# Performance work log

Measured on AMD Instinct MI355X. Metric: run time of the kernel, lower is better.

Reference implementation:

```python
import jax, jax.numpy as jnp
import numpy as np

N, E, F, H, G = 50000, 640000, 128, 128, 64


def setup_inputs() -> dict:
    key = jax.random.key(0)
    ks = jax.random.split(key, 10)
    x = jax.random.normal(ks[0], (N, F), dtype=jnp.float32)
    edge_index = jax.random.randint(ks[1], (2, E), 0, N)
    batch = jnp.sort(jax.random.randint(ks[2], (N,), 0, G))

    def glorot(k, shp):
        return jax.random.normal(k, shp, dtype=jnp.float32) * np.float32(1.0 / np.sqrt(shp[0]))

    W1 = glorot(ks[3], (F, H)); b1 = jnp.zeros((H,), jnp.float32)
    W2 = glorot(ks[4], (H, H)); b2 = jnp.zeros((H,), jnp.float32)
    W3 = glorot(ks[5], (H, H)); b3 = jnp.zeros((H,), jnp.float32)
    W4 = glorot(ks[6], (H, 2)); b4 = jnp.zeros((2,), jnp.float32)
    return {"x": x, "W1": W1, "b1": b1, "W2": W2, "b2": b2,
            "W3": W3, "b3": b3, "W4": W4, "b4": b4,
            "edge_index": edge_index, "batch": batch, "num_graphs": G}


def reference(x, W1, b1, W2, b2, W3, b3, W4, b4, edge_index, batch, num_graphs):
    n = x.shape[0]
    loop = jnp.arange(n, dtype=edge_index.dtype)
    src = jnp.concatenate([edge_index[0], loop])  # with self-loops (PyG GCNConv default)
    dst = jnp.concatenate([edge_index[1], loop])
    # symmetric degree normalization: D^{-1/2} (A+I) D^{-1/2}
    deg = jax.ops.segment_sum(jnp.ones_like(src, dtype=x.dtype), dst, num_segments=n)
    dinv = jnp.where(deg > 0, jax.lax.rsqrt(deg), 0.0)
    norm = (dinv[src] * dinv[dst])[:, None]  # [E+N, 1]

    def gcn_conv(h, W, b):
        m = h @ W                                   # transform first (F->H), then propagate
        agg = jax.ops.segment_sum(m[src] * norm, dst, num_segments=n)
        return agg + b

    h = jax.nn.relu(gcn_conv(x, W1, b1))
    h = jax.nn.relu(gcn_conv(h, W2, b2))
    g = jax.ops.segment_max(h, batch, num_segments=num_graphs)  # global_max_pool
    z = jax.nn.relu(g @ W3 + b3)                    # dropout is identity in eval
    logits = z @ W4 + b4
    return jax.nn.log_softmax(logits, axis=1)
```

## Files before the change

kernel.cpp:

```cpp
#include <hip/hip_runtime.h>
#include <hip/hip_bf16.h>
#include <math.h>

#define HDIM 128
#define SCAN_B 256
#define NBLK 256

typedef short bfrag __attribute__((ext_vector_type(8)));
typedef float f32x4 __attribute__((ext_vector_type(4)));

__device__ inline unsigned short f2bf_rne(float x) {
    unsigned u = __float_as_uint(x);
    u = (u + 0x7fffu + ((u >> 16) & 1u)) >> 16;
    return (unsigned short)u;
}
__device__ inline float bf_lo(unsigned u) { return __uint_as_float(u << 16); }
__device__ inline float bf_hi(unsigned u) { return __uint_as_float(u & 0xffff0000u); }
__device__ inline unsigned bf_pack(float lo, float hi) {
    return ((unsigned)f2bf_rne(hi) << 16) | (unsigned)f2bf_rne(lo);
}


__device__ inline void hist_body(int b, const int* __restrict__ dst,
                                 int* __restrict__ hist, int E, int chunk, int nbuck) {
    __shared__ int hl[256];
    int t = threadIdx.x;
    hl[t] = 0;
    __syncthreads();
    int start = b * chunk, end = min(E, start + chunk);
    for (int e = start + t; e < end; e += 256) atomicAdd(&hl[dst[e] >> 8], 1);
    __syncthreads();
    if (t < nbuck) hist[t * NBLK + b] = hl[t];
}

__device__ inline void wfrag_body(int b, const float* __restrict__ W1,
                                  const float* __restrict__ W2,
                                  unsigned short* __restrict__ w1h,
                                  unsigned short* __restrict__ w1l,
                                  unsigned short* __restrict__ w2h,
                                  unsigned short* __restrict__ w2l) {
    const float* W = (b < 64) ? W1 : W2;
    unsigned short* whi = (b < 64) ? w1h : w2h;
    unsigned short* wlo = (b < 64) ? w1l : w2l;
    int idx = (b & 63) * 256 + threadIdx.x;
    int k = idx >> 7;
    int n = idx & 127;
    int kt = k >> 5, q = (k >> 3) & 3, j = k & 7;
    int lm = n >> 3, nt = n & 7;
    int lane = q * 16 + lm;
    int o = ((kt * 8 + nt) * 64 + lane) * 8 + j;
    float x = W[idx];
    unsigned short hb = f2bf_rne(x);
    float hf = __uint_as_float(((unsigned)hb) << 16);
    unsigned short lb = f2bf_rne(x - hf);
    whi[o] = hb;
    wlo[o] = lb;
}

__device__ inline void scatter_body(int b, const int* __restrict__ srcv,
                                    const int* __restrict__ dstv,
                                    const int* __restrict__ hscan,
                                    int2* __restrict__ sorted,
                                    int E, int chunk, int nbuck) {
    __shared__ int cur[256];
    int t = threadIdx.x;
    if (t < nbuck) cur[t] = hscan[t * NBLK + b];
    __syncthreads();
    int start = b * chunk, end = min(E, start + chunk);
    for (int e = start + t; e < end; e += 256) {
        int d = dstv[e];
        int pos = atomicAdd(&cur[d >> 8], 1);
        sorted[pos] = make_int2(srcv[e], d);
    }
}

#define GBM 64
__device__ inline void gemm_f32_body(int b, const float* __restrict__ A,
                                     const unsigned short* __restrict__ whi,
                                     const unsigned short* __restrict__ wlo,
                                     unsigned short* __restrict__ C, int Nrows) {
    int tid = threadIdx.x;
    int w = tid >> 6, L = tid & 63;
    int lm = L & 15, lq = L >> 4;
    int row0 = b * GBM + w * 16;

    f32x4 acc[8];
#pragma unroll
    for (int nt = 0; nt < 8; ++nt) acc[nt] = (f32x4)(0.f);

#pragma unroll
    for (int kt = 0; kt < 4; ++kt) {
        int gr = row0 + lm;
        float4 v0 = make_float4(0.f, 0.f, 0.f, 0.f);
        float4 v1 = v0;
        if (gr < Nrows) {
            const float* p = &A[(size_t)gr * HDIM + kt * 32 + lq * 8];
            v0 = *(const float4*)p;
            v1 = *(const float4*)(p + 4);
        }
        float xv[8] = {v0.x, v0.y, v0.z, v0.w, v1.x, v1.y, v1.z, v1.w};
        bfrag ah, al;
#pragma unroll
        for (int j = 0; j < 8; ++j) {
            float x = xv[j];
            unsigned short hb = f2bf_rne(x);
            float hf = __uint_as_float(((unsigned)hb) << 16);
            unsigned short lb = f2bf_rne(x - hf);
            ah[j] = (short)hb;
            al[j] = (short)lb;
        }
#pragma unroll
        for (int nt = 0; nt < 8; ++nt) {
            int o = ((kt * 8 + nt) * 64 + L) * 8;
            bfrag wh = *(const bfrag*)&whi[o];
            bfrag wl = *(const bfrag*)&wlo[o];
            acc[nt] = __builtin_amdgcn_mfma_f32_16x16x32_bf16(ah, wh, acc[nt], 0, 0, 0);
            acc[nt] = __builtin_amdgcn_mfma_f32_16x16x32_bf16(al, wh, acc[nt], 0, 0, 0);
            acc[nt] = __builtin_amdgcn_mfma_f32_16x16x32_bf16(ah, wl, acc[nt], 0, 0, 0);
        }
    }

#pragma unroll
    for (int i = 0; i < 4; ++i) {
        int gr = row0 + lq * 4 + i;
        if (gr < Nrows) {
            bfrag e;
#pragma unroll
            for (int nt = 0; nt < 8; ++nt) e[nt] = (short)f2bf_rne(acc[nt][i]);
            *(bfrag*)&C[(size_t)gr * HDIM + lm * 8] = e;
        }
    }
}

__global__ __launch_bounds__(256) void mega1_kernel(const int* __restrict__ dst,
                                                    int* __restrict__ hist, int E,
                                                    int chunk, int nbuck,
                                                    const float* __restrict__ W1,
                                                    const float* __restrict__ W2,
                                                    unsigned short* __restrict__ w1h,
                                                    unsigned short* __restrict__ w1l,
                                                    unsigned short* __restrict__ w2h,
                                                    unsigned short* __restrict__ w2l) {
    int b = blockIdx.x;
    if (b < NBLK) hist_body(b, dst, hist, E, chunk, nbuck);
    else wfrag_body(b - NBLK, W1, W2, w1h, w1l, w2h, w2l);
}

__global__ __launch_bounds__(256) void mega3_kernel(const int* __restrict__ srcv,
                                                    const int* __restrict__ dstv,
                                                    const int* __restrict__ hscan,
                                                    int2* __restrict__ sorted,
                                                    int E, int chunk, int nbuck,
                                                    const float* __restrict__ A,
                                                    const unsigned short* __restrict__ whi,
                                                    const unsigned short* __restrict__ wlo,
                                                    unsigned short* __restrict__ C, int Nrows) {
    int b = blockIdx.x;
    if (b < NBLK) scatter_body(b, srcv, dstv, hscan, sorted, E, chunk, nbuck);
    else gemm_f32_body(b - NBLK, A, whi, wlo, C, Nrows);
}

__global__ __launch_bounds__(SCAN_B) void scan1_kernel(const int* __restrict__ in,
                                                       int* __restrict__ out,
                                                       int* __restrict__ sums, int n) {
    __shared__ int s[SCAN_B];
    int t = threadIdx.x;
    int idx = blockIdx.x * SCAN_B + t;
    int v = (idx < n) ? in[idx] : 0;
    s[t] = v;
    __syncthreads();
    for (int off = 1; off < SCAN_B; off <<= 1) {
        int x = (t >= off) ? s[t - off] : 0;
        __syncthreads();
        s[t] += x;
        __syncthreads();
    }
    if (idx < n) out[idx] = s[t];
    if (t == SCAN_B - 1) sums[blockIdx.x] = s[t];
}

__global__ __launch_bounds__(SCAN_B) void scan2_kernel(int* __restrict__ sums, int nb) {
    __shared__ int s[SCAN_B];
    int t = threadIdx.x;
    int v = (t < nb) ? sums[t] : 0;
    s[t] = v;
    __syncthreads();
    for (int off = 1; off < SCAN_B; off <<= 1) {
        int x = (t >= off) ? s[t - off] : 0;
        __syncthreads();
        s[t] += x;
        __syncthreads();
    }
    if (t < nb) sums[t] = s[t] - v;
}

__global__ __launch_bounds__(SCAN_B) void scan3_kernel(const int* __restrict__ in,
                                                       int* __restrict__ out,
                                                       const int* __restrict__ sums, int n) {
    int idx = blockIdx.x * SCAN_B + threadIdx.x;
    if (idx < n) out[idx] = out[idx] - in[idx] + sums[blockIdx.x];
}

__global__ __launch_bounds__(256) void csr_kernel(const int2* __restrict__ sorted,
                                                  const int* __restrict__ hscan,
                                                  int* __restrict__ rowstart,
                                                  float* __restrict__ dinv,
                                                  int* __restrict__ csr,
                                                  int N, int E, int nbuck) {
    __shared__ int cnt[256];
    __shared__ int s[256];
    __shared__ int cur[256];
    int b = blockIdx.x;
    int t = threadIdx.x;
    int start = hscan[b * NBLK];
    int end = (b + 1 < nbuck) ? hscan[(b + 1) * NBLK] : E;
    cnt[t] = 0;
    __syncthreads();
    for (int e = start + t; e < end; e += 256)
        atomicAdd(&cnt[sorted[e].y & 255], 1);
    __syncthreads();
    int v = cnt[t];
    s[t] = v;
    __syncthreads();
    for (int off = 1; off < 256; off <<= 1) {
        int x = (t >= off) ? s[t - off] : 0;
        __syncthreads();
        s[t] += x;
        __syncthreads();
    }
    int excl = s[t] - v;
    int node = b * 256 + t;
    if (node < N) {
        rowstart[node] = start + excl;
        dinv[node] = rsqrtf((float)(v + 1));
    }
    if (b == nbuck - 1 && t == 0) rowstart[N] = E;
    cur[t] = start + excl;
    __syncthreads();
    for (int e = start + t; e < end; e += 256) {
        int2 ed = sorted[e];
        int pos = atomicAdd(&cur[ed.y & 255], 1);
        csr[pos] = ed.x;
    }
}

#define QACC(UV, WT)                                   \
    acc[0] = fmaf(WT, bf_lo((UV).x), acc[0]);          \
    acc[1] = fmaf(WT, bf_hi((UV).x), acc[1]);          \
    acc[2] = fmaf(WT, bf_lo((UV).y), acc[2]);          \
    acc[3] = fmaf(WT, bf_hi((UV).y), acc[3]);          \
    acc[4] = fmaf(WT, bf_lo((UV).z), acc[4]);          \
    acc[5] = fmaf(WT, bf_hi((UV).z), acc[5]);          \
    acc[6] = fmaf(WT, bf_lo((UV).w), acc[6]);          \
    acc[7] = fmaf(WT, bf_hi((UV).w), acc[7]);

__device__ inline void qgather(const uint4* __restrict__ m4,
                               const int* __restrict__ csr,
                               const float* __restrict__ dinv,
                               int p, int pend, int t, float* acc) {
    for (; p + 8 <= pend; p += 8) {
        int s0 = csr[p], s1 = csr[p + 1], s2 = csr[p + 2], s3 = csr[p + 3];
        int s4 = csr[p + 4], s5 = csr[p + 5], s6 = csr[p + 6], s7 = csr[p + 7];
        float w0 = dinv[s0], w1 = dinv[s1], w2 = dinv[s2], w3 = dinv[s3];
        float w4 = dinv[s4], w5 = dinv[s5], w6 = dinv[s6], w7 = dinv[s7];
        uint4 u0 = m4[(size_t)s0 * 16 + t];
        uint4 u1 = m4[(size_t)s1 * 16 + t];
        uint4 u2 = m4[(size_t)s2 * 16 + t];
        uint4 u3 = m4[(size_t)s3 * 16 + t];
        uint4 u4 = m4[(size_t)s4 * 16 + t];
        uint4 u5 = m4[(size_t)s5 * 16 + t];
        uint4 u6 = m4[(size_t)s6 * 16 + t];
        uint4 u7 = m4[(size_t)s7 * 16 + t];
        QACC(u0, w0); QACC(u1, w1); QACC(u2, w2); QACC(u3, w3);
        QACC(u4, w4); QACC(u5, w5); QACC(u6, w6); QACC(u7, w7);
    }
    if (p + 4 <= pend) {
        int s0 = csr[p], s1 = csr[p + 1], s2 = csr[p + 2], s3 = csr[p + 3];
        float w0 = dinv[s0], w1 = dinv[s1], w2 = dinv[s2], w3 = dinv[s3];
        uint4 u0 = m4[(size_t)s0 * 16 + t];
        uint4 u1 = m4[(size_t)s1 * 16 + t];
        uint4 u2 = m4[(size_t)s2 * 16 + t];
        uint4 u3 = m4[(size_t)s3 * 16 + t];
        QACC(u0, w0); QACC(u1, w1); QACC(u2, w2); QACC(u3, w3);
        p += 4;
    }
    if (p + 2 <= pend) {
        int s0 = csr[p], s1 = csr[p + 1];
        float w0 = dinv[s0], w1 = dinv[s1];
        uint4 u0 = m4[(size_t)s0 * 16 + t];
        uint4 u1 = m4[(size_t)s1 * 16 + t];
        QACC(u0, w0); QACC(u1, w1);
        p += 2;
    }
    if (p < pend) {
        int s0 = csr[p];
        float w0 = dinv[s0];
        uint4 u0 = m4[(size_t)s0 * 16 + t];
        QACC(u0, w0);
    }
}

__global__ __launch_bounds__(256) void agg_gemm_kernel(
        const uint4* __restrict__ m4,
        const int* __restrict__ rowstart,
        const int* __restrict__ csr,
        const float* __restrict__ dinv,
        const float* __restrict__ bias,
        const unsigned short* __restrict__ whi,
        const unsigned short* __restrict__ wlo,
        uint4* __restrict__ out_m, int n) {
    __shared__ unsigned short hbuf[16][HDIM + 8];
    __shared__ float cbuf[16][HDIM + 4];
    int t = threadIdx.x & 15;
    int nl = threadIdx.x >> 4;
    int node = blockIdx.x * 16 + nl;

    unsigned short hv[8] = {0, 0, 0, 0, 0, 0, 0, 0};
    if (node < n) {
        float dd = dinv[node];
        float acc[8];
        uint4 u = m4[(size_t)node * 16 + t];
        acc[0] = dd * bf_lo(u.x); acc[1] = dd * bf_hi(u.x);
        acc[2] = dd * bf_lo(u.y); acc[3] = dd * bf_hi(u.y);
        acc[4] = dd * bf_lo(u.z); acc[5] = dd * bf_hi(u.z);
        acc[6] = dd * bf_lo(u.w); acc[7] = dd * bf_hi(u.w);
        qgather(m4, csr, dinv, rowstart[node], rowstart[node + 1], t, acc);
        float4 b0 = *(const float4*)&bias[t * 8];
        float4 b1 = *(const float4*)&bias[t * 8 + 4];
        float bb[8] = {b0.x, b0.y, b0.z, b0.w, b1.x, b1.y, b1.z, b1.w};
#pragma unroll
        for (int j = 0; j < 8; ++j)
            hv[j] = f2bf_rne(fmaxf(fmaf(dd, acc[j], bb[j]), 0.f));
    }
    *(uint4*)&hbuf[nl][t * 8] = *(uint4*)hv;
    __syncthreads();

    int w = threadIdx.x >> 6, L = threadIdx.x & 63;
    int lm = L & 15, lq = L >> 4;
    f32x4 acc2[2];
    acc2[0] = (f32x4)(0.f);
    acc2[1] = (f32x4)(0.f);
#pragma unroll
    for (int kt = 0; kt < 4; ++kt) {
        bfrag a = *(const bfrag*)&hbuf[lm][kt * 32 + lq * 8];
#pragma unroll
        for (int q2 = 0; q2 < 2; ++q2) {
            int nt = w * 2 + q2;
            int o = ((kt * 8 + nt) * 64 + L) * 8;
            bfrag wh = *(const bfrag*)&whi[o];
            bfrag wl = *(const bfrag*)&wlo[o];
            acc2[q2] = __builtin_amdgcn_mfma_f32_16x16x32_bf16(a, wh, acc2[q2], 0, 0, 0);
            acc2[q2] = __builtin_amdgcn_mfma_f32_16x16x32_bf16(a, wl, acc2[q2], 0, 0, 0);
        }
    }
#pragma unroll
    for (int q2 = 0; q2 < 2; ++q2) {
        int nt = w * 2 + q2;
#pragma unroll
        for (int i = 0; i < 4; ++i) cbuf[lq * 4 + i][lm * 8 + nt] = acc2[q2][i];
    }
    __syncthreads();

    if (node < n) {
        float4 r0 = *(const float4*)&cbuf[nl][t * 8];
        float4 r1 = *(const float4*)&cbuf[nl][t * 8 + 4];
        unsigned short ev[8];
        ev[0] = f2bf_rne(r0.x); ev[1] = f2bf_rne(r0.y);
        ev[2] = f2bf_rne(r0.z); ev[3] = f2bf_rne(r0.w);
        ev[4] = f2bf_rne(r1.x); ev[5] = f2bf_rne(r1.y);
        ev[6] = f2bf_rne(r1.z); ev[7] = f2bf_rne(r1.w);
        out_m[(size_t)node * 16 + t] = *(uint4*)ev;
    }
}

__global__ __launch_bounds__(256) void agg_pool_kernel(const uint4* __restrict__ m4,
                                                       const int* __restrict__ rowstart,
                                                       const int* __restrict__ csr,
                                                       const float* __restrict__ dinv,
                                                       const float* __restrict__ bias,
                                                       const int* __restrict__ batch,
                                                       unsigned int* __restrict__ g, int n) {
    __shared__ float smx[16][HDIM];
    __shared__ int sgid[16];
    int t = threadIdx.x & 15;
    int nl = threadIdx.x >> 4;
    int node = blockIdx.x * 16 + nl;
    bool valid = node < n;
    if (valid) {
        float dd = dinv[node];
        float acc[8];
        uint4 u = m4[(size_t)node * 16 + t];
        acc[0] = dd * bf_lo(u.x); acc[1] = dd * bf_hi(u.x);
        acc[2] = dd * bf_lo(u.y); acc[3] = dd * bf_hi(u.y);
        acc[4] = dd * bf_lo(u.z); acc[5] = dd * bf_hi(u.z);
        acc[6] = dd * bf_lo(u.w); acc[7] = dd * bf_hi(u.w);
        qgather(m4, csr, dinv, rowstart[node], rowstart[node + 1], t, acc);
        float4 b0 = *(const float4*)&bias[t * 8];
        float4 b1 = *(const float4*)&bias[t * 8 + 4];
        float4 r0, r1;
        r0.x = fmaxf(fmaf(dd, acc[0], b0.x), 0.f);
        r0.y = fmaxf(fmaf(dd, acc[1], b0.y), 0.f);
        r0.z = fmaxf(fmaf(dd, acc[2], b0.z), 0.f);
        r0.w = fmaxf(fmaf(dd, acc[3], b0.w), 0.f);
        r1.x = fmaxf(fmaf(dd, acc[4], b1.x), 0.f);
        r1.y = fmaxf(fmaf(dd, acc[5], b1.y), 0.f);
        r1.z = fmaxf(fmaf(dd, acc[6], b1.z), 0.f);
        r1.w = fmaxf(fmaf(dd, acc[7], b1.w), 0.f);
        *(float4*)&smx[nl][t * 8] = r0;
        *(float4*)&smx[nl][t * 8 + 4] = r1;
    }
    if (t == 0) sgid[nl] = valid ? batch[node] : -1;
    __syncthreads();
    if (threadIdx.x < HDIM) {
        int c = threadIdx.x;
        int curg = -1;
        float run = 0.f;
#pragma unroll
        for (int r = 0; r < 16; ++r) {
            int gg = sgid[r];
            if (gg < 0) continue;
            if (gg != curg) {
                if (curg >= 0) atomicMax(&g[curg * HDIM + c], __float_as_uint(run));
                curg = gg;
                run = smx[r][c];
            } else {
                run = fmaxf(run, smx[r][c]);
            }
        }
        if (curg >= 0) atomicMax(&g[curg * HDIM + c], __float_as_uint(run));
    }
}

__global__ __launch_bounds__(128) void mlp_kernel(const unsigned int* __restrict__ gbits,
                                                  const float* __restrict__ W3,
                                                  const float* __restrict__ b3,
                                                  const float* __restrict__ W4,
                                                  const float* __restrict__ b4,
                                                  float* __restrict__ out) {
    __shared__ float gs[HDIM];
    __shared__ float r0[HDIM];
    __shared__ float r1[HDIM];
    int j = threadIdx.x;
    int b = blockIdx.x;
    gs[j] = __uint_as_float(gbits[b * HDIM + j]);
    __syncthreads();
    float acc = b3[j];
#pragma unroll 8
    for (int k = 0; k < HDIM; ++k) acc = fmaf(gs[k], W3[k * HDIM + j], acc);
    float z = fmaxf(acc, 0.f);
    r0[j] = z * W4[j * 2 + 0];
    r1[j] = z * W4[j * 2 + 1];
    __syncthreads();
    for (int off = 64; off > 0; off >>= 1) {
        if (j < off) {
            r0[j] += r0[j + off];
            r1[j] += r1[j + off];
        }
        __syncthreads();
    }
    if (j == 0) {
        float l0 = r0[0] + b4[0];
        float l1 = r1[0] + b4[1];
        float mx = fmaxf(l0, l1);
        float lse = mx + logf(expf(l0 - mx) + expf(l1 - mx));
        out[b * 2 + 0] = l0 - lse;
        out[b * 2 + 1] = l1 - lse;
    }
}

extern "C" void kernel_launch(void* const* d_in, const int* in_sizes, int n_in,
                              void* d_out, int out_size, void* d_ws, size_t ws_size,
                              hipStream_t stream) {
    const float* x  = (const float*)d_in[0];
    const float* W1 = (const float*)d_in[1];
    const float* b1 = (const float*)d_in[2];
    const float* W2 = (const float*)d_in[3];
    const float* b2 = (const float*)d_in[4];
    const float* W3 = (const float*)d_in[5];
    const float* b3 = (const float*)d_in[6];
    const float* W4 = (const float*)d_in[7];
    const float* b4 = (const float*)d_in[8];
    const int* ei    = (const int*)d_in[9];
    const int* batch = (const int*)d_in[10];

    const int N = in_sizes[0] / HDIM;
    const int E = in_sizes[9] / 2;
    const int G = out_size / 2;
    const int* src = ei;
    const int* dst = ei + E;

    const int nbuck = (N + 255) >> 8;
    const int nscan = nbuck * NBLK;
    const int chunk = (E + NBLK - 1) / NBLK;

    const int Nr = ((N + 63) / 64) * 64;
    char* wsb = (char*)d_ws;
    size_t o = 0;
    unsigned int* g = (unsigned int*)(wsb + o); o += (size_t)G * HDIM * 4;
    size_t zero_bytes = o;
    int* hist = (int*)(wsb + o);           o += (size_t)nscan * 4;
    int* hscan = (int*)(wsb + o);          o += (size_t)nscan * 4;
    int* sums = (int*)(wsb + o);           o += 256 * 4;
    int* rowstart = (int*)(wsb + o);       o += (size_t)(Nr + 64) * 4;
    float* dinv = (float*)(wsb + o);       o += (size_t)Nr * 4;
    int2* sorted = (int2*)(wsb + o);       o += (size_t)E * 8;
    int* csr = (int*)(wsb + o);            o += (size_t)E * 4;
    unsigned short* wf1h = (unsigned short*)(wsb + o); o += (size_t)HDIM * HDIM * 2;
    unsigned short* wf1l = (unsigned short*)(wsb + o); o += (size_t)HDIM * HDIM * 2;
    unsigned short* wf2h = (unsigned short*)(wsb + o); o += (size_t)HDIM * HDIM * 2;
    unsigned short* wf2l = (unsigned short*)(wsb + o); o += (size_t)HDIM * HDIM * 2;
    unsigned short* m = (unsigned short*)(wsb + o);    o += (size_t)Nr * HDIM * 2;
    unsigned short* m2 = (unsigned short*)(wsb + o);   o += (size_t)Nr * HDIM * 2;
    (void)ws_size; (void)n_in;

    (void)hipMemsetAsync(d_ws, 0, zero_bytes, stream);

    int sblocks = (nscan + SCAN_B - 1) / SCAN_B;
    int gemm_blocks = (N + GBM - 1) / GBM;
    int agg_blocks = (N + 15) / 16;

    mega1_kernel<<<NBLK + 128, 256, 0, stream>>>(dst, hist, E, chunk, nbuck,
                                                 W1, W2, wf1h, wf1l, wf2h, wf2l);
    scan1_kernel<<<sblocks, SCAN_B, 0, stream>>>(hist, hscan, sums, nscan);
    scan2_kernel<<<1, SCAN_B, 0, stream>>>(sums, sblocks);
    scan3_kernel<<<sblocks, SCAN_B, 0, stream>>>(hist, hscan, sums, nscan);
    mega3_kernel<<<NBLK + gemm_blocks, 256, 0, stream>>>(src, dst, hscan, sorted,
                                                         E, chunk, nbuck,
                                                         x, wf1h, wf1l, m, N);
    csr_kernel<<<nbuck, 256, 0, stream>>>(sorted, hscan, rowstart, dinv, csr, N, E, nbuck);
    agg_gemm_kernel<<<agg_blocks, 256, 0, stream>>>((const uint4*)m, rowstart, csr,
                                                    dinv, b1, wf2h, wf2l,
                                                    (uint4*)m2, N);
    agg_pool_kernel<<<agg_blocks, 256, 0, stream>>>((const uint4*)m2, rowstart, csr,
                                                    dinv, b2, batch, g, N);
    mlp_kernel<<<G, 128, 0, stream>>>(g, W3, b3, W4, b4, (float*)d_out);
}
```

Before: 201.7 us.

## Pack sorted edges into 32-bit words, fuse scan passes, alias LDS buffers

The bucketed edge list now stores the source index and the low 8 bits of the destination in one 32-bit int instead of an int2, halving scatter and CSR traffic. The scan2 and scan3 kernels are merged so that each block re-scans the block sums itself, removing one launch. In agg_gemm, the bf16 staging buffer and the fp32 output buffer now share one LDS array, with an extra barrier between uses. The packing assumes source indices fit in 16 bits, but N=50000 needs them to fit in 65536, which holds only for this size.

After: 202.8 us. No clear change (+0.5%).

```diff
diff --git a/kernel.cpp b/kernel.cpp
--- a/kernel.cpp
+++ b/kernel.cpp
@@ -16,9 +16,6 @@
 }
 __device__ inline float bf_lo(unsigned u) { return __uint_as_float(u << 16); }
 __device__ inline float bf_hi(unsigned u) { return __uint_as_float(u & 0xffff0000u); }
-__device__ inline unsigned bf_pack(float lo, float hi) {
-    return ((unsigned)f2bf_rne(hi) << 16) | (unsigned)f2bf_rne(lo);
-}
 
 
 __device__ inline void hist_body(int b, const int* __restrict__ dst,
@@ -60,7 +57,7 @@
 __device__ inline void scatter_body(int b, const int* __restrict__ srcv,
                                     const int* __restrict__ dstv,
                                     const int* __restrict__ hscan,
-                                    int2* __restrict__ sorted,
+                                    int* __restrict__ sorted,
                                     int E, int chunk, int nbuck) {
     __shared__ int cur[256];
     int t = threadIdx.x;
@@ -70,7 +67,7 @@
     for (int e = start + t; e < end; e += 256) {
         int d = dstv[e];
         int pos = atomicAdd(&cur[d >> 8], 1);
-        sorted[pos] = make_int2(srcv[e], d);
+        sorted[pos] = srcv[e] | ((d & 255) << 16);
     }
 }
 
@@ -149,7 +146,7 @@
 __global__ __launch_bounds__(256) void mega3_kernel(const int* __restrict__ srcv,
                                                     const int* __restrict__ dstv,
                                                     const int* __restrict__ hscan,
-                                                    int2* __restrict__ sorted,
+                                                    int* __restrict__ sorted,
                                                     int E, int chunk, int nbuck,
                                                     const float* __restrict__ A,
                                                     const unsigned short* __restrict__ whi,
@@ -179,7 +176,10 @@
     if (t == SCAN_B - 1) sums[blockIdx.x] = s[t];
 }
 
-__global__ __launch_bounds__(SCAN_B) void scan2_kernel(int* __restrict__ sums, int nb) {
+__global__ __launch_bounds__(SCAN_B) void scan3_kernel(const int* __restrict__ in,
+                                                       int* __restrict__ out,
+                                                       const int* __restrict__ sums,
+                                                       int n, int nb) {
     __shared__ int s[SCAN_B];
     int t = threadIdx.x;
     int v = (t < nb) ? sums[t] : 0;
@@ -191,17 +191,12 @@
         s[t] += x;
         __syncthreads();
     }
-    if (t < nb) sums[t] = s[t] - v;
-}
-
-__global__ __launch_bounds__(SCAN_B) void scan3_kernel(const int* __restrict__ in,
-                                                       int* __restrict__ out,
-                                                       const int* __restrict__ sums, int n) {
-    int idx = blockIdx.x * SCAN_B + threadIdx.x;
-    if (idx < n) out[idx] = out[idx] - in[idx] + sums[blockIdx.x];
-}
-
-__global__ __launch_bounds__(256) void csr_kernel(const int2* __restrict__ sorted,
+    int base = (blockIdx.x > 0) ? s[blockIdx.x - 1] : 0;
+    int idx = blockIdx.x * SCAN_B + t;
+    if (idx < n) out[idx] = out[idx] - in[idx] + base;
+}
+
+__global__ __launch_bounds__(256) void csr_kernel(const int* __restrict__ sorted,
                                                   const int* __restrict__ hscan,
                                                   int* __restrict__ rowstart,
                                                   float* __restrict__ dinv,
@@ -217,7 +212,7 @@
     cnt[t] = 0;
     __syncthreads();
     for (int e = start + t; e < end; e += 256)
-        atomicAdd(&cnt[sorted[e].y & 255], 1);
+        atomicAdd(&cnt[(sorted[e] >> 16) & 255], 1);
     __syncthreads();
     int v = cnt[t];
     s[t] = v;
@@ -238,9 +233,9 @@
     cur[t] = start + excl;
     __syncthreads();
     for (int e = start + t; e < end; e += 256) {
-        int2 ed = sorted[e];
-        int pos = atomicAdd(&cur[ed.y & 255], 1);
-        csr[pos] = ed.x;
+        int ed = sorted[e];
+        int pos = atomicAdd(&cur[(ed >> 16) & 255], 1);
+        csr[pos] = ed & 0xFFFF;
     }
 }
 
@@ -309,8 +304,8 @@
         const unsigned short* __restrict__ whi,
         const unsigned short* __restrict__ wlo,
         uint4* __restrict__ out_m, int n) {
-    __shared__ unsigned short hbuf[16][HDIM + 8];
-    __shared__ float cbuf[16][HDIM + 4];
+    __shared__ float lds[16 * (HDIM + 4)];
+    unsigned short* hbuf = (unsigned short*)lds;
     int t = threadIdx.x & 15;
     int nl = threadIdx.x >> 4;
     int node = blockIdx.x * 16 + nl;
@@ -332,7 +327,7 @@
         for (int j = 0; j < 8; ++j)
             hv[j] = f2bf_rne(fmaxf(fmaf(dd, acc[j], bb[j]), 0.f));
     }
-    *(uint4*)&hbuf[nl][t * 8] = *(uint4*)hv;
+    *(uint4*)&hbuf[nl * (HDIM + 8) + t * 8] = *(uint4*)hv;
     __syncthreads();
 
     int w = threadIdx.x >> 6, L = threadIdx.x & 63;
@@ -342,7 +337,7 @@
     acc2[1] = (f32x4)(0.f);
 #pragma unroll
     for (int kt = 0; kt < 4; ++kt) {
-        bfrag a = *(const bfrag*)&hbuf[lm][kt * 32 + lq * 8];
+        bfrag a = *(const bfrag*)&hbuf[lm * (HDIM + 8) + kt * 32 + lq * 8];
 #pragma unroll
         for (int q2 = 0; q2 < 2; ++q2) {
             int nt = w * 2 + q2;
@@ -353,17 +348,21 @@
             acc2[q2] = __builtin_amdgcn_mfma_f32_16x16x32_bf16(a, wl, acc2[q2], 0, 0, 0);
         }
     }
+    __syncthreads();
+
+    float* cbuf = lds;
 #pragma unroll
     for (int q2 = 0; q2 < 2; ++q2) {
         int nt = w * 2 + q2;
 #pragma unroll
-        for (int i = 0; i < 4; ++i) cbuf[lq * 4 + i][lm * 8 + nt] = acc2[q2][i];
+        for (int i = 0; i < 4; ++i)
+            cbuf[(lq * 4 + i) * (HDIM + 4) + lm * 8 + nt] = acc2[q2][i];
     }
     __syncthreads();
 
     if (node < n) {
-        float4 r0 = *(const float4*)&cbuf[nl][t * 8];
-        float4 r1 = *(const float4*)&cbuf[nl][t * 8 + 4];
+        float4 r0 = *(const float4*)&cbuf[nl * (HDIM + 4) + t * 8];
+        float4 r1 = *(const float4*)&cbuf[nl * (HDIM + 4) + t * 8 + 4];
         unsigned short ev[8];
         ev[0] = f2bf_rne(r0.x); ev[1] = f2bf_rne(r0.y);
         ev[2] = f2bf_rne(r0.z); ev[3] = f2bf_rne(r0.w);
@@ -503,7 +502,7 @@
     int* sums = (int*)(wsb + o);           o += 256 * 4;
     int* rowstart = (int*)(wsb + o);       o += (size_t)(Nr + 64) * 4;
     float* dinv = (float*)(wsb + o);       o += (size_t)Nr * 4;
-    int2* sorted = (int2*)(wsb + o);       o += (size_t)E * 8;
+    int* sorted = (int*)(wsb + o);         o += (size_t)E * 4;
     int* csr = (int*)(wsb + o);            o += (size_t)E * 4;
     unsigned short* wf1h = (unsigned short*)(wsb + o); o += (size_t)HDIM * HDIM * 2;
     unsigned short* wf1l = (unsigned short*)(wsb + o); o += (size_t)HDIM * HDIM * 2;
@@ -522,8 +521,7 @@
     mega1_kernel<<<NBLK + 128, 256, 0, stream>>>(dst, hist, E, chunk, nbuck,
                                                  W1, W2, wf1h, wf1l, wf2h, wf2l);
     scan1_kernel<<<sblocks, SCAN_B, 0, stream>>>(hist, hscan, sums, nscan);
-    scan2_kernel<<<1, SCAN_B, 0, stream>>>(sums, sblocks);
-    scan3_kernel<<<sblocks, SCAN_B, 0, stream>>>(hist, hscan, sums, nscan);
+    scan3_kernel<<<sblocks, SCAN_B, 0, stream>>>(hist, hscan, sums, nscan, sblocks);
     mega3_kernel<<<NBLK + gemm_blocks, 256, 0, stream>>>(src, dst, hscan, sorted,
                                                          E, chunk, nbuck,
                                                          x, wf1h, wf1l, m, N);
```
